# Kernel optimization log

Measured on AMD Instinct MI355X. Metric: run time of the kernel, lower is better.

## Reference

```python
import jax, jax.numpy as jnp
import numpy as np

B, S, HID, NH = 2, 2048, 2048, 16
HD = HID // NH  # head_dim = 128


def setup_inputs() -> dict:
    key = jax.random.key(0)
    ks = jax.random.split(key, 10)
    sc = 1.0 / np.sqrt(HID)
    inp = {
        "hidden_state": jax.random.normal(ks[0], (B, S, HID), dtype=jnp.float32),
        # upper-triangular (strict) causal mask: 1 where attention is forbidden
        "casual_mask": jnp.triu(jnp.ones((S, S), dtype=jnp.float32), k=1),
        # pad last 128 tokens of each sequence
        "pad_mask": jnp.concatenate(
            [jnp.zeros((B, S - 128), jnp.float32), jnp.ones((B, 128), jnp.float32)], axis=1
        ),
        # weights stored [in, out] (transposed vs torch Linear)
        "Wq": jax.random.normal(ks[1], (HID, HID), dtype=jnp.float32) * sc,
        "bq": jnp.zeros((HID,), jnp.float32),
        "Wk": jax.random.normal(ks[2], (HID, HD), dtype=jnp.float32) * sc,
        "bk": jnp.zeros((HD,), jnp.float32),
        "Wv": jax.random.normal(ks[3], (HID, HD), dtype=jnp.float32) * sc,
        "bv": jnp.zeros((HD,), jnp.float32),
        "Wo": jax.random.normal(ks[4], (HID, HID), dtype=jnp.float32) * sc,
        "bo": jnp.zeros((HID,), jnp.float32),
    }
    return inp


def reference(hidden_state, casual_mask, pad_mask, Wq, bq, Wk, bk, Wv, bv, Wo, bo):
    bsz, seq_len, hid = hidden_state.shape
    nh = NH
    hd = hid // nh
    q = hidden_state @ Wq + bq                      # [B,S,HID]
    k = hidden_state @ Wk + bk                      # [B,S,HD]  single shared head
    v = hidden_state @ Wv + bv                      # [B,S,HD]
    q = q.reshape(bsz, seq_len, nh, hd).transpose(0, 2, 1, 3)  # [B,NH,S,HD]
    # attn scores: shared K broadcast across all query heads
    scores = jnp.einsum("bhqd,bkd->bhqk", q, k) / jnp.sqrt(jnp.float32(hd))
    scores = scores + casual_mask * (-1e9)
    scores = scores + pad_mask[:, None, None, :] * (-1e9)
    probs = jax.nn.softmax(scores, axis=-1)         # [B,NH,S,S]
    out = jnp.einsum("bhqk,bkd->bhqd", probs, v)    # [B,NH,S,HD]
    out = out.transpose(0, 2, 1, 3).reshape(bsz, seq_len, hid)
    return out @ Wo + bo
```

## Files before the change

### kernel.cpp

```cpp
#include <hip/hip_runtime.h>
#include <hip/hip_bf16.h>
#include <math.h>

#define B_    2
#define S_    2048
#define HID_  2048
#define NH_   16
#define HD_   128
#define MTOT  4096
#define QKV_N 2304

typedef short bf16x8 __attribute__((ext_vector_type(8)));
typedef float f32x4  __attribute__((ext_vector_type(4)));
typedef float f32x16 __attribute__((ext_vector_type(16)));

__device__ __forceinline__ ushort f2bf(float f) {
    __hip_bfloat16 h = __float2bfloat16(f);
    ushort u; __builtin_memcpy(&u, &h, 2); return u;
}

__device__ __forceinline__ uint cvtpk_bf16(float lo, float hi) {
    uint r;
    asm("v_cvt_pk_bf16_f32 %0, %1, %2" : "=v"(r) : "v"(lo), "v"(hi));
    return r;
}

__device__ __forceinline__ void gload_lds16(const void* g, void* l) {
    __builtin_amdgcn_global_load_lds(
        (const __attribute__((address_space(1))) void*)g,
        (__attribute__((address_space(3))) void*)l, 16, 0, 0);
}

__global__ void prep(const float* __restrict__ hidden, ushort* __restrict__ hbf,
                     const float* __restrict__ Wq, const float* __restrict__ Wk,
                     const float* __restrict__ Wv, const float* __restrict__ Wo,
                     ushort* __restrict__ WqkvT, ushort* __restrict__ WoT,
                     const float* __restrict__ bq, const float* __restrict__ bk,
                     const float* __restrict__ bv, float* __restrict__ bqkv,
                     int* __restrict__ ctr)
{
    __shared__ float tile[32][33];
    const int bid = blockIdx.x;
    const int tid = threadIdx.x;

    if (bid < 4096) {
        long i = ((long)bid * 256 + tid) * 8;
        float4 a = *(const float4*)&hidden[i];
        float4 b = *(const float4*)&hidden[i + 4];
        uint4 o;
        o.x = (uint)f2bf(a.x) | ((uint)f2bf(a.y) << 16);
        o.y = (uint)f2bf(a.z) | ((uint)f2bf(a.w) << 16);
        o.z = (uint)f2bf(b.x) | ((uint)f2bf(b.y) << 16);
        o.w = (uint)f2bf(b.z) | ((uint)f2bf(b.w) << 16);
        *(uint4*)&hbf[i] = o;
        return;
    }
    if (bid >= 12800) {
        int i = (bid - 12800) * 256 + tid;
        if (i == 0) *ctr = 0;
        if (i < 2048)      bqkv[i] = bq[i];
        else if (i < 2176) bqkv[i] = bk[i - 2048];
        else if (i < QKV_N) bqkv[i] = bv[i - 2176];
        return;
    }

    const float* W; ushort* T; int N, rowoff, r;
    if (bid < 8192)      { W = Wq; T = WqkvT; N = 2048; rowoff = 0;    r = bid - 4096; }
    else if (bid < 8448) { W = Wk; T = WqkvT; N = 128;  rowoff = 2048; r = bid - 8192; }
    else if (bid < 8704) { W = Wv; T = WqkvT; N = 128;  rowoff = 2176; r = bid - 8448; }
    else                 { W = Wo; T = WoT;   N = 2048; rowoff = 0;    r = bid - 8704; }
    const int nxt = N >> 5;
    const int bx = r % nxt, by = r / nxt;
    const int tx = tid & 31, ty = tid >> 5;
    const int n0 = bx * 32, k0 = by * 32;
#pragma unroll
    for (int i = 0; i < 4; i++)
        tile[ty + 8 * i][tx] = W[(long)(k0 + ty + 8 * i) * N + n0 + tx];
    __syncthreads();
#pragma unroll
    for (int i = 0; i < 4; i++)
        T[(long)(rowoff + n0 + ty + 8 * i) * 2048 + k0 + tx] = f2bf(tile[tx][ty + 8 * i]);
}

__global__ __launch_bounds__(256, 3) void gemm_qkv(
    const ushort* __restrict__ A, const ushort* __restrict__ Bt,
    const float* __restrict__ bias,
    ushort* __restrict__ qbuf, ushort* __restrict__ kbuf,
    ushort* __restrict__ vtbuf)
{
    const int K = HID_;
    __shared__ __align__(16) ushort As[2 * 128 * 32];
    __shared__ __align__(16) ushort Bs[2 * 128 * 32];
    const int t = threadIdx.x;
    const int w = t >> 6, l = t & 63;
    const long bm = (long)blockIdx.y * 128;
    const long bn = (long)blockIdx.x * 128;

    f32x4 acc[4][4];
#pragma unroll
    for (int i = 0; i < 4; i++)
#pragma unroll
        for (int j = 0; j < 4; j++) acc[i][j] = (f32x4){0.f, 0.f, 0.f, 0.f};

    const int srow = w * 16 + (l >> 2);
    const int scol = (l & 3) * 8;
    const ushort* Ag0 = A + (bm + srow) * (long)K + scol;
    const ushort* Ag1 = A + (bm + srow + 64) * (long)K + scol;
    const ushort* Bg0 = Bt + (bn + srow) * (long)K + scol;
    const ushort* Bg1 = Bt + (bn + srow + 64) * (long)K + scol;
    ushort* Al0 = As + w * 512;
    ushort* Al1 = As + 2048 + w * 512;
    ushort* Bl0 = Bs + w * 512;
    ushort* Bl1 = Bs + 2048 + w * 512;

    const int mrow = l & 15, kq = l >> 4;
    const int moff = (w & 1) * 64, noff = (w >> 1) * 64;

    gload_lds16(Ag0, Al0);
    gload_lds16(Ag1, Al1);
    gload_lds16(Bg0, Bl0);
    gload_lds16(Bg1, Bl1);
    __syncthreads();

    for (int k0 = 0; k0 < K; k0 += 32) {
        const int cb = (k0 >> 5) & 1;
        const int po = cb * 4096;
        if (k0 + 32 < K) {
            const int pn = (cb ^ 1) * 4096;
            gload_lds16(Ag0 + k0 + 32, Al0 + pn);
            gload_lds16(Ag1 + k0 + 32, Al1 + pn);
            gload_lds16(Bg0 + k0 + 32, Bl0 + pn);
            gload_lds16(Bg1 + k0 + 32, Bl1 + pn);
        }
        bf16x8 af[4], bfr[4];
#pragma unroll
        for (int i = 0; i < 4; i++)
            af[i] = *(const bf16x8*)&As[po + (moff + i * 16 + mrow) * 32 + kq * 8];
#pragma unroll
        for (int j = 0; j < 4; j++)
            bfr[j] = *(const bf16x8*)&Bs[po + (noff + j * 16 + mrow) * 32 + kq * 8];
#pragma unroll
        for (int i = 0; i < 4; i++)
#pragma unroll
            for (int j = 0; j < 4; j++)
                acc[i][j] = __builtin_amdgcn_mfma_f32_16x16x32_bf16(
                    af[i], bfr[j], acc[i][j], 0, 0, 0);
        __syncthreads();
    }

    const int crow = (l >> 4) * 4, ccol = l & 15;
    const int tile = blockIdx.x;
#pragma unroll
    for (int i = 0; i < 4; i++) {
#pragma unroll
        for (int j = 0; j < 4; j++) {
            long colg = bn + noff + j * 16 + ccol;
            float bv = bias[colg];
            long row0 = bm + moff + i * 16 + crow;
            float v[4];
#pragma unroll
            for (int r = 0; r < 4; r++) v[r] = acc[i][j][r] + bv;
            if (tile < 16) {
#pragma unroll
                for (int r = 0; r < 4; r++)
                    qbuf[(row0 + r) * (long)HID_ + colg] = f2bf(v[r]);
            } else if (tile == 16) {
                long ck = colg - 2048;
#pragma unroll
                for (int r = 0; r < 4; r++)
                    kbuf[(row0 + r) * (long)HD_ + ck] = f2bf(v[r]);
            } else {
                long cv = colg - 2176;
                long b  = row0 >> 11;
                long s0 = row0 & 2047;
                ushort4 pk;
                pk.x = f2bf(v[0]); pk.y = f2bf(v[1]);
                pk.z = f2bf(v[2]); pk.w = f2bf(v[3]);
                *(ushort4*)&vtbuf[b * (HD_ * (long)S_) + cv * (long)S_ + s0] = pk;
            }
        }
    }
}

__global__ __launch_bounds__(256, 3) void gemm_mfma(
    const ushort* __restrict__ A, const ushort* __restrict__ Bt,
    const float* __restrict__ bias, float* __restrict__ C,
    int K, int ldc)
{
    __shared__ __align__(16) ushort As[2 * 128 * 32];
    __shared__ __align__(16) ushort Bs[2 * 128 * 32];
    const int t = threadIdx.x;
    const int w = t >> 6, l = t & 63;
    const long bm = (long)blockIdx.y * 128;
    const long bn = (long)blockIdx.x * 128;

    f32x4 acc[4][4];
#pragma unroll
    for (int i = 0; i < 4; i++)
#pragma unroll
        for (int j = 0; j < 4; j++) acc[i][j] = (f32x4){0.f, 0.f, 0.f, 0.f};

    const int srow = w * 16 + (l >> 2);
    const int scol = (l & 3) * 8;
    const ushort* Ag0 = A + (bm + srow) * (long)K + scol;
    const ushort* Ag1 = A + (bm + srow + 64) * (long)K + scol;
    const ushort* Bg0 = Bt + (bn + srow) * (long)K + scol;
    const ushort* Bg1 = Bt + (bn + srow + 64) * (long)K + scol;
    ushort* Al0 = As + w * 512;
    ushort* Al1 = As + 2048 + w * 512;
    ushort* Bl0 = Bs + w * 512;
    ushort* Bl1 = Bs + 2048 + w * 512;

    const int mrow = l & 15, kq = l >> 4;
    const int moff = (w & 1) * 64, noff = (w >> 1) * 64;

    gload_lds16(Ag0, Al0);
    gload_lds16(Ag1, Al1);
    gload_lds16(Bg0, Bl0);
    gload_lds16(Bg1, Bl1);
    __syncthreads();

    for (int k0 = 0; k0 < K; k0 += 32) {
        const int cb = (k0 >> 5) & 1;
        const int po = cb * 4096;
        if (k0 + 32 < K) {
            const int pn = (cb ^ 1) * 4096;
            gload_lds16(Ag0 + k0 + 32, Al0 + pn);
            gload_lds16(Ag1 + k0 + 32, Al1 + pn);
            gload_lds16(Bg0 + k0 + 32, Bl0 + pn);
            gload_lds16(Bg1 + k0 + 32, Bl1 + pn);
        }
        bf16x8 af[4], bfr[4];
#pragma unroll
        for (int i = 0; i < 4; i++)
            af[i] = *(const bf16x8*)&As[po + (moff + i * 16 + mrow) * 32 + kq * 8];
#pragma unroll
        for (int j = 0; j < 4; j++)
            bfr[j] = *(const bf16x8*)&Bs[po + (noff + j * 16 + mrow) * 32 + kq * 8];
#pragma unroll
        for (int i = 0; i < 4; i++)
#pragma unroll
            for (int j = 0; j < 4; j++)
                acc[i][j] = __builtin_amdgcn_mfma_f32_16x16x32_bf16(
                    af[i], bfr[j], acc[i][j], 0, 0, 0);
        __syncthreads();
    }

    const int crow = (l >> 4) * 4, ccol = l & 15;
#pragma unroll
    for (int i = 0; i < 4; i++) {
#pragma unroll
        for (int j = 0; j < 4; j++) {
            long col = bn + noff + j * 16 + ccol;
            float bv = bias[col];
#pragma unroll
            for (int r = 0; r < 4; r++) {
                long row = bm + moff + i * 16 + crow + r;
                C[row * (long)ldc + col] = acc[i][j][r] + bv;
            }
        }
    }
}

__global__ __launch_bounds__(512, 1) void attn_mfma(
    const ushort* __restrict__ qbuf, const ushort* __restrict__ kbuf,
    const ushort* __restrict__ vtbuf, ushort* __restrict__ outp,
    int* __restrict__ workctr)
{
    __shared__ __align__(16) char smem[86016];
    ushort* KsB = (ushort*)smem;
    ushort* VtB = (ushort*)(smem + 32768);
    float*  OP  = (float*)smem;
    float*  LP  = (float*)(smem + 65536);
    int*    sidx = (int*)(smem + 66048);

    const int t = threadIdx.x, w = t >> 6, l = t & 63;
    const int wq = w & 3, kh = w >> 2;
    const int l31 = l & 31, h5 = l >> 5;

    int koff[2], klo[2], voff[2], vlo[2];
#pragma unroll
    for (int i = 0; i < 2; i++) {
        const int c = w * 2 + i;
        const int key0 = c * 4 + (l >> 4);
        const int gk = (l & 15) ^ (key0 & 15);
        koff[i] = key0 * HD_ + gk * 8;
        klo[i]  = c * 512 + l * 8;
        const int d = c * 8 + (l >> 3);
        const int gv = (l & 7) ^ (d & 7);
        voff[i] = d * S_ + gv * 8;
        vlo[i]  = c * 512 + l * 8;
    }

    const float SC = 0.08838834764831845f * 1.44269504089f;

    for (;;) {
        if (t == 0) *sidx = atomicAdd(workctr, 1);
        __syncthreads();
        const int idx = *sidx;
        if (idx >= 512) break;

        const int qblk = 15 - (idx >> 5);
        const int hb = idx & 31;
        const int h = hb & 15, b = hb >> 4;
        const long rowbase = (long)b * S_;
        const int qbase = qblk * 128 + wq * 32;
        const int qmaxw = qbase + 31;
        int kTiles = 2 * qblk + 2;
        if (kTiles > 30) kTiles = 30;
        const ushort* kb0 = kbuf + rowbase * (long)HD_;
        const ushort* vb0 = vtbuf + (long)b * (HD_ * (long)S_);

        bf16x8 qf[8];
        {
            const ushort* qp = qbuf + (rowbase + qbase + l31) * (long)HID_
                                    + h * HD_ + h5 * 8;
#pragma unroll
            for (int ks = 0; ks < 8; ks++) qf[ks] = *(const bf16x8*)(qp + ks * 16);
        }

        f32x16 o[4] = {};
        float lrun = 0.f;

#pragma unroll
        for (int i = 0; i < 2; i++) {
            gload_lds16(kb0 + koff[i], KsB + klo[i]);
            gload_lds16(vb0 + voff[i], VtB + vlo[i]);
        }
        __syncthreads();

        for (int kt = 0; kt < kTiles; kt++) {
            const int cur = kt & 1;
            const int ktb = kt * 64;

            if (kt + 1 < kTiles) {
                const int nxt = cur ^ 1;
                const int nb = ktb + 64;
#pragma unroll
                for (int i = 0; i < 2; i++) {
                    gload_lds16(kb0 + koff[i] + (long)nb * HD_,
                                KsB + nxt * 8192 + klo[i]);
                    gload_lds16(vb0 + voff[i] + nb, VtB + nxt * 8192 + vlo[i]);
                }
            }

            if (ktb <= qmaxw) {
                const ushort* Ks = KsB + cur * 8192;
                const ushort* Vt = VtB + cur * 8192;

                f32x16 c0 = {};
                const int key = kh * 32 + l31;
#pragma unroll
                for (int ks = 0; ks < 8; ks++) {
                    const int g = (ks * 2 + h5) ^ (key & 15);
                    bf16x8 a = *(const bf16x8*)&Ks[key * 128 + g * 8];
                    c0 = __builtin_amdgcn_mfma_f32_32x32x16_bf16(
                        a, qf[ks], c0, 0, 0, 0);
                }

                const bool boundary = (ktb + 63 > qbase) || (ktb >= S_ - 128);
                if (boundary) {
                    const int qg = qbase + l31;
#pragma unroll
                    for (int g = 0; g < 4; g++)
#pragma unroll
                        for (int r = 0; r < 4; r++) {
                            const int keyg = ktb + kh * 32 + 4 * h5 + 8 * g + r;
                            if (keyg > qg || keyg >= S_ - 128)
                                c0[g * 4 + r] = -3.0e38f;
                        }
                }

                float s0 = 0.f, s1 = 0.f, s2 = 0.f, s3 = 0.f;
#pragma unroll
                for (int g = 0; g < 4; g++) {
                    float p0 = __builtin_amdgcn_exp2f(c0[g * 4 + 0] * SC);
                    float p1 = __builtin_amdgcn_exp2f(c0[g * 4 + 1] * SC);
                    float p2 = __builtin_amdgcn_exp2f(c0[g * 4 + 2] * SC);
                    float p3 = __builtin_amdgcn_exp2f(c0[g * 4 + 3] * SC);
                    c0[g * 4 + 0] = p0; s0 += p0;
                    c0[g * 4 + 1] = p1; s1 += p1;
                    c0[g * 4 + 2] = p2; s2 += p2;
                    c0[g * 4 + 3] = p3; s3 += p3;
                }
                float sum = (s0 + s1) + (s2 + s3);
                sum += __shfl_xor(sum, 32);
                lrun += sum;

#pragma unroll
                for (int j = 0; j < 2; j++) {
                    const int base = j * 8;
                    uint X  = cvtpk_bf16(c0[base + 0], c0[base + 1]);
                    uint Y  = cvtpk_bf16(c0[base + 2], c0[base + 3]);
                    uint Z  = cvtpk_bf16(c0[base + 4], c0[base + 5]);
                    uint Wd = cvtpk_bf16(c0[base + 6], c0[base + 7]);
                    asm("v_permlane32_swap_b32 %0, %1" : "+v"(X), "+v"(Z));
                    asm("v_permlane32_swap_b32 %0, %1" : "+v"(Y), "+v"(Wd));
                    uint tmp[4] = {X, Y, Z, Wd};
                    bf16x8 pf;
                    __builtin_memcpy(&pf, tmp, 16);
                    const int ks2 = kh * 2 + j;
#pragma unroll
                    for (int mb = 0; mb < 4; mb++) {
                        const int d = mb * 32 + l31;
                        const int g = (ks2 * 2 + h5) ^ (d & 7);
                        bf16x8 a = *(const bf16x8*)&Vt[d * 64 + g * 8];
                        o[mb] = __builtin_amdgcn_mfma_f32_32x32x16_bf16(
                            a, pf, o[mb], 0, 0, 0);
                    }
                }
            }
            __syncthreads();
        }

        if (kh == 1) {
#pragma unroll
            for (int mb = 0; mb < 4; mb++)
#pragma unroll
                for (int r = 0; r < 16; r++) {
                    const int d = mb * 32 + (r & 3) + 8 * (r >> 2) + 4 * h5;
                    OP[wq * 4096 + d * 32 + l31] = o[mb][r];
                }
            LP[wq * 32 + l31] = lrun;
        }
        __syncthreads();
        if (kh == 0) {
#pragma unroll
            for (int mb = 0; mb < 4; mb++)
#pragma unroll
                for (int r = 0; r < 16; r++) {
                    const int d = mb * 32 + (r & 3) + 8 * (r >> 2) + 4 * h5;
                    o[mb][r] += OP[wq * 4096 + d * 32 + l31];
                }
            lrun += LP[wq * 32 + l31];
        }
        __syncthreads();

        if (kh == 0) {
            ushort* Ob = (ushort*)smem + wq * 4352;
            const float inv = 1.f / lrun;
#pragma unroll
            for (int mb = 0; mb < 4; mb++) {
#pragma unroll
                for (int g = 0; g < 4; g++) {
                    const int d0 = mb * 32 + 4 * h5 + 8 * g;
                    ushort4 pk;
                    pk.x = f2bf(o[mb][g * 4 + 0] * inv);
                    pk.y = f2bf(o[mb][g * 4 + 1] * inv);
                    pk.z = f2bf(o[mb][g * 4 + 2] * inv);
                    pk.w = f2bf(o[mb][g * 4 + 3] * inv);
                    *(ushort4*)&Ob[l31 * 136 + d0] = pk;
                }
            }
            __builtin_amdgcn_s_waitcnt(0);
            const int q = l >> 1, half = l & 1;
            const ushort* src = Ob + q * 136 + half * 64;
            ushort* dst = outp + (rowbase + qblk * 128 + wq * 32 + q) * (long)HID_
                               + h * HD_ + half * 64;
#pragma unroll
            for (int i = 0; i < 8; i++) {
                uint4 v = *(const uint4*)(src + i * 8);
                *(uint4*)(dst + i * 8) = v;
            }
        }
    }
}

extern "C" void kernel_launch(void* const* d_in, const int* in_sizes, int n_in,
                              void* d_out, int out_size, void* d_ws, size_t ws_size,
                              hipStream_t stream)
{
    const float* hidden = (const float*)d_in[0];
    const float* Wq  = (const float*)d_in[3];
    const float* bq  = (const float*)d_in[4];
    const float* Wk  = (const float*)d_in[5];
    const float* bk  = (const float*)d_in[6];
    const float* Wv  = (const float*)d_in[7];
    const float* bv  = (const float*)d_in[8];
    const float* Wo  = (const float*)d_in[9];
    const float* bo  = (const float*)d_in[10];
    float* out = (float*)d_out;

    char* ws = (char*)d_ws;
    ushort* hbf   = (ushort*)(ws);
    ushort* WqkvT = (ushort*)(ws + 16777216);
    ushort* WoT   = (ushort*)(ws + 26214400);
    float*  bqkv  = (float*) (ws + 34603008);
    int*    wctr  = (int*)   (ws + 34612224);
    ushort* qbuf  = (ushort*)(ws + 34619392);
    ushort* kbuf  = (ushort*)(ws + 51396608);
    ushort* vtbuf = (ushort*)(ws + 52445184);
    ushort* attnO = (ushort*)(ws + 53493760);

    prep<<<12809, 256, 0, stream>>>(hidden, hbf, Wq, Wk, Wv, Wo,
                                    WqkvT, WoT, bq, bk, bv, bqkv, wctr);
    gemm_qkv<<<dim3(18, 32), 256, 0, stream>>>(hbf, WqkvT, bqkv,
                                               qbuf, kbuf, vtbuf);
    attn_mfma<<<256, 512, 0, stream>>>(qbuf, kbuf, vtbuf, attnO, wctr);
    gemm_mfma<<<dim3(16, 32), 256, 0, stream>>>(attnO, WoT, bo, out,
                                                HID_, HID_);
}
```

Baseline: 285.7 us.

## Replace persistent atomic work queue in attention with static grid and two blocks per CU

```diff
diff --git a/kernel.cpp b/kernel.cpp
--- a/kernel.cpp
+++ b/kernel.cpp
@@ -36,8 +36,7 @@
                      const float* __restrict__ Wv, const float* __restrict__ Wo,
                      ushort* __restrict__ WqkvT, ushort* __restrict__ WoT,
                      const float* __restrict__ bq, const float* __restrict__ bk,
-                     const float* __restrict__ bv, float* __restrict__ bqkv,
-                     int* __restrict__ ctr)
+                     const float* __restrict__ bv, float* __restrict__ bqkv)
 {
     __shared__ float tile[32][33];
     const int bid = blockIdx.x;
@@ -57,7 +56,6 @@
     }
     if (bid >= 12800) {
         int i = (bid - 12800) * 256 + tid;
-        if (i == 0) *ctr = 0;
         if (i < 2048)      bqkv[i] = bq[i];
         else if (i < 2176) bqkv[i] = bk[i - 2048];
         else if (i < QKV_N) bqkv[i] = bv[i - 2176];
@@ -262,21 +260,32 @@
     }
 }
 
-__global__ __launch_bounds__(512, 1) void attn_mfma(
+__global__ __launch_bounds__(512) __attribute__((amdgpu_waves_per_eu(4, 4)))
+void attn_mfma(
     const ushort* __restrict__ qbuf, const ushort* __restrict__ kbuf,
-    const ushort* __restrict__ vtbuf, ushort* __restrict__ outp,
-    int* __restrict__ workctr)
+    const ushort* __restrict__ vtbuf, ushort* __restrict__ outp)
 {
-    __shared__ __align__(16) char smem[86016];
+    __shared__ __align__(16) char smem[66048];
     ushort* KsB = (ushort*)smem;
     ushort* VtB = (ushort*)(smem + 32768);
     float*  OP  = (float*)smem;
     float*  LP  = (float*)(smem + 65536);
-    int*    sidx = (int*)(smem + 66048);
 
     const int t = threadIdx.x, w = t >> 6, l = t & 63;
     const int wq = w & 3, kh = w >> 2;
     const int l31 = l & 31, h5 = l >> 5;
+
+    const int bid = blockIdx.x;
+    const int qblk = (bid < 256) ? (15 - (bid >> 5)) : ((bid - 256) >> 5);
+    const int hb = bid & 31;
+    const int h = hb & 15, b = hb >> 4;
+    const long rowbase = (long)b * S_;
+    const int qbase = qblk * 128 + wq * 32;
+    const int qmaxw = qbase + 31;
+    int kTiles = 2 * qblk + 2;
+    if (kTiles > 30) kTiles = 30;
+    const ushort* kb0 = kbuf + rowbase * (long)HD_;
+    const ushort* vb0 = vtbuf + (long)b * (HD_ * (long)S_);
 
     int koff[2], klo[2], voff[2], vlo[2];
 #pragma unroll
@@ -294,174 +303,156 @@
 
     const float SC = 0.08838834764831845f * 1.44269504089f;
 
-    for (;;) {
-        if (t == 0) *sidx = atomicAdd(workctr, 1);
+    bf16x8 qf[8];
+    {
+        const ushort* qp = qbuf + (rowbase + qbase + l31) * (long)HID_
+                                + h * HD_ + h5 * 8;
+#pragma unroll
+        for (int ks = 0; ks < 8; ks++) qf[ks] = *(const bf16x8*)(qp + ks * 16);
+    }
+
+    f32x16 o[4] = {};
+    float lrun = 0.f;
+
+#pragma unroll
+    for (int i = 0; i < 2; i++) {
+        gload_lds16(kb0 + koff[i], KsB + klo[i]);
+        gload_lds16(vb0 + voff[i], VtB + vlo[i]);
+    }
+    __syncthreads();
+
+    for (int kt = 0; kt < kTiles; kt++) {
+        const int cur = kt & 1;
+        const int ktb = kt * 64;
+
+        if (kt + 1 < kTiles) {
+            const int nxt = cur ^ 1;
+            const int nb = ktb + 64;
+#pragma unroll
+            for (int i = 0; i < 2; i++) {
+                gload_lds16(kb0 + koff[i] + (long)nb * HD_,
+                            KsB + nxt * 8192 + klo[i]);
+                gload_lds16(vb0 + voff[i] + nb, VtB + nxt * 8192 + vlo[i]);
+            }
+        }
+
+        if (ktb <= qmaxw) {
+            const ushort* Ks = KsB + cur * 8192;
+            const ushort* Vt = VtB + cur * 8192;
+
+            f32x16 c0 = {};
+            const int key = kh * 32 + l31;
+#pragma unroll
+            for (int ks = 0; ks < 8; ks++) {
+                const int g = (ks * 2 + h5) ^ (key & 15);
+                bf16x8 a = *(const bf16x8*)&Ks[key * 128 + g * 8];
+                c0 = __builtin_amdgcn_mfma_f32_32x32x16_bf16(
+                    a, qf[ks], c0, 0, 0, 0);
+            }
+
+            const bool boundary = (ktb + 63 > qbase);
+            if (boundary) {
+                const int qg = qbase + l31;
+#pragma unroll
+                for (int g = 0; g < 4; g++)
+#pragma unroll
+                    for (int r = 0; r < 4; r++) {
+                        const int keyg = ktb + kh * 32 + 4 * h5 + 8 * g + r;
+                        if (keyg > qg)
+                            c0[g * 4 + r] = -3.0e38f;
+                    }
+            }
+
+            float s0 = 0.f, s1 = 0.f, s2 = 0.f, s3 = 0.f;
+#pragma unroll
+            for (int g = 0; g < 4; g++) {
+                float p0 = __builtin_amdgcn_exp2f(c0[g * 4 + 0] * SC);
+                float p1 = __builtin_amdgcn_exp2f(c0[g * 4 + 1] * SC);
+                float p2 = __builtin_amdgcn_exp2f(c0[g * 4 + 2] * SC);
+                float p3 = __builtin_amdgcn_exp2f(c0[g * 4 + 3] * SC);
+                c0[g * 4 + 0] = p0; s0 += p0;
+                c0[g * 4 + 1] = p1; s1 += p1;
+                c0[g * 4 + 2] = p2; s2 += p2;
+                c0[g * 4 + 3] = p3; s3 += p3;
+            }
+            float sum = (s0 + s1) + (s2 + s3);
+            sum += __shfl_xor(sum, 32);
+            lrun += sum;
+
+#pragma unroll
+            for (int j = 0; j < 2; j++) {
+                const int base = j * 8;
+                uint X  = cvtpk_bf16(c0[base + 0], c0[base + 1]);
+                uint Y  = cvtpk_bf16(c0[base + 2], c0[base + 3]);
+                uint Z  = cvtpk_bf16(c0[base + 4], c0[base + 5]);
+                uint Wd = cvtpk_bf16(c0[base + 6], c0[base + 7]);
+                asm("v_permlane32_swap_b32 %0, %1" : "+v"(X), "+v"(Z));
+                asm("v_permlane32_swap_b32 %0, %1" : "+v"(Y), "+v"(Wd));
+                uint tmp[4] = {X, Y, Z, Wd};
+                bf16x8 pf;
+                __builtin_memcpy(&pf, tmp, 16);
+                const int ks2 = kh * 2 + j;
+#pragma unroll
+                for (int mb = 0; mb < 4; mb++) {
+                    const int d = mb * 32 + l31;
+                    const int g = (ks2 * 2 + h5) ^ (d & 7);
+                    bf16x8 a = *(const bf16x8*)&Vt[d * 64 + g * 8];
+                    o[mb] = __builtin_amdgcn_mfma_f32_32x32x16_bf16(
+                        a, pf, o[mb], 0, 0, 0);
+                }
+            }
+        }
         __syncthreads();
-        const int idx = *sidx;
-        if (idx >= 512) break;
-
-        const int qblk = 15 - (idx >> 5);
-        const int hb = idx & 31;
-        const int h = hb & 15, b = hb >> 4;
-        const long rowbase = (long)b * S_;
-        const int qbase = qblk * 128 + wq * 32;
-        const int qmaxw = qbase + 31;
-        int kTiles = 2 * qblk + 2;
-        if (kTiles > 30) kTiles = 30;
-        const ushort* kb0 = kbuf + rowbase * (long)HD_;
-        const ushort* vb0 = vtbuf + (long)b * (HD_ * (long)S_);
-
-        bf16x8 qf[8];
-        {
-            const ushort* qp = qbuf + (rowbase + qbase + l31) * (long)HID_
-                                    + h * HD_ + h5 * 8;
-#pragma unroll
-            for (int ks = 0; ks < 8; ks++) qf[ks] = *(const bf16x8*)(qp + ks * 16);
-        }
-
-        f32x16 o[4] = {};
-        float lrun = 0.f;
-
-#pragma unroll
-        for (int i = 0; i < 2; i++) {
-            gload_lds16(kb0 + koff[i], KsB + klo[i]);
-            gload_lds16(vb0 + voff[i], VtB + vlo[i]);
-        }
-        __syncthreads();
-
-        for (int kt = 0; kt < kTiles; kt++) {
-            const int cur = kt & 1;
-            const int ktb = kt * 64;
-
-            if (kt + 1 < kTiles) {
-                const int nxt = cur ^ 1;
-                const int nb = ktb + 64;
-#pragma unroll
-                for (int i = 0; i < 2; i++) {
-                    gload_lds16(kb0 + koff[i] + (long)nb * HD_,
-                                KsB + nxt * 8192 + klo[i]);
-                    gload_lds16(vb0 + voff[i] + nb, VtB + nxt * 8192 + vlo[i]);
-                }
-            }
-
-            if (ktb <= qmaxw) {
-                const ushort* Ks = KsB + cur * 8192;
-                const ushort* Vt = VtB + cur * 8192;
-
-                f32x16 c0 = {};
-                const int key = kh * 32 + l31;
-#pragma unroll
-                for (int ks = 0; ks < 8; ks++) {
-                    const int g = (ks * 2 + h5) ^ (key & 15);
-                    bf16x8 a = *(const bf16x8*)&Ks[key * 128 + g * 8];
-                    c0 = __builtin_amdgcn_mfma_f32_32x32x16_bf16(
-                        a, qf[ks], c0, 0, 0, 0);
-                }
-
-                const bool boundary = (ktb + 63 > qbase) || (ktb >= S_ - 128);
-                if (boundary) {
-                    const int qg = qbase + l31;
-#pragma unroll
-                    for (int g = 0; g < 4; g++)
-#pragma unroll
-                        for (int r = 0; r < 4; r++) {
-                            const int keyg = ktb + kh * 32 + 4 * h5 + 8 * g + r;
-                            if (keyg > qg || keyg >= S_ - 128)
-                                c0[g * 4 + r] = -3.0e38f;
-                        }
-                }
-
-                float s0 = 0.f, s1 = 0.f, s2 = 0.f, s3 = 0.f;
-#pragma unroll
-                for (int g = 0; g < 4; g++) {
-                    float p0 = __builtin_amdgcn_exp2f(c0[g * 4 + 0] * SC);
-                    float p1 = __builtin_amdgcn_exp2f(c0[g * 4 + 1] * SC);
-                    float p2 = __builtin_amdgcn_exp2f(c0[g * 4 + 2] * SC);
-                    float p3 = __builtin_amdgcn_exp2f(c0[g * 4 + 3] * SC);
-                    c0[g * 4 + 0] = p0; s0 += p0;
-                    c0[g * 4 + 1] = p1; s1 += p1;
-                    c0[g * 4 + 2] = p2; s2 += p2;
-                    c0[g * 4 + 3] = p3; s3 += p3;
-                }
-                float sum = (s0 + s1) + (s2 + s3);
-                sum += __shfl_xor(sum, 32);
-                lrun += sum;
-
-#pragma unroll
-                for (int j = 0; j < 2; j++) {
-                    const int base = j * 8;
-                    uint X  = cvtpk_bf16(c0[base + 0], c0[base + 1]);
-                    uint Y  = cvtpk_bf16(c0[base + 2], c0[base + 3]);
-                    uint Z  = cvtpk_bf16(c0[base + 4], c0[base + 5]);
-                    uint Wd = cvtpk_bf16(c0[base + 6], c0[base + 7]);
-                    asm("v_permlane32_swap_b32 %0, %1" : "+v"(X), "+v"(Z));
-                    asm("v_permlane32_swap_b32 %0, %1" : "+v"(Y), "+v"(Wd));
-                    uint tmp[4] = {X, Y, Z, Wd};
-                    bf16x8 pf;
-                    __builtin_memcpy(&pf, tmp, 16);
-                    const int ks2 = kh * 2 + j;
-#pragma unroll
-                    for (int mb = 0; mb < 4; mb++) {
-                        const int d = mb * 32 + l31;
-                        const int g = (ks2 * 2 + h5) ^ (d & 7);
-                        bf16x8 a = *(const bf16x8*)&Vt[d * 64 + g * 8];
-                        o[mb] = __builtin_amdgcn_mfma_f32_32x32x16_bf16(
-                            a, pf, o[mb], 0, 0, 0);
-                    }
-                }
-            }
-            __syncthreads();
-        }
-
-        if (kh == 1) {
-#pragma unroll
-            for (int mb = 0; mb < 4; mb++)
-#pragma unroll
-                for (int r = 0; r < 16; r++) {
-                    const int d = mb * 32 + (r & 3) + 8 * (r >> 2) + 4 * h5;
-                    OP[wq * 4096 + d * 32 + l31] = o[mb][r];
-                }
-            LP[wq * 32 + l31] = lrun;
-        }
-        __syncthreads();
-        if (kh == 0) {
-#pragma unroll
-            for (int mb = 0; mb < 4; mb++)
-#pragma unroll
-                for (int r = 0; r < 16; r++) {
-                    const int d = mb * 32 + (r & 3) + 8 * (r >> 2) + 4 * h5;
-                    o[mb][r] += OP[wq * 4096 + d * 32 + l31];
-                }
-            lrun += LP[wq * 32 + l31];
-        }
-        __syncthreads();
-
-        if (kh == 0) {
-            ushort* Ob = (ushort*)smem + wq * 4352;
-            const float inv = 1.f / lrun;
-#pragma unroll
-            for (int mb = 0; mb < 4; mb++) {
-#pragma unroll
-                for (int g = 0; g < 4; g++) {
-                    const int d0 = mb * 32 + 4 * h5 + 8 * g;
-                    ushort4 pk;
-                    pk.x = f2bf(o[mb][g * 4 + 0] * inv);
-                    pk.y = f2bf(o[mb][g * 4 + 1] * inv);
-                    pk.z = f2bf(o[mb][g * 4 + 2] * inv);
-                    pk.w = f2bf(o[mb][g * 4 + 3] * inv);
-                    *(ushort4*)&Ob[l31 * 136 + d0] = pk;
-                }
-            }
-            __builtin_amdgcn_s_waitcnt(0);
-            const int q = l >> 1, half = l & 1;
-            const ushort* src = Ob + q * 136 + half * 64;
-            ushort* dst = outp + (rowbase + qblk * 128 + wq * 32 + q) * (long)HID_
-                               + h * HD_ + half * 64;
-#pragma unroll
-            for (int i = 0; i < 8; i++) {
-                uint4 v = *(const uint4*)(src + i * 8);
-                *(uint4*)(dst + i * 8) = v;
-            }
+    }
+
+    if (kh == 1) {
+#pragma unroll
+        for (int mb = 0; mb < 4; mb++)
+#pragma unroll
+            for (int r = 0; r < 16; r++) {
+                const int d = mb * 32 + (r & 3) + 8 * (r >> 2) + 4 * h5;
+                OP[wq * 4096 + d * 32 + l31] = o[mb][r];
+            }
+        LP[wq * 32 + l31] = lrun;
+    }
+    __syncthreads();
+    if (kh == 0) {
+#pragma unroll
+        for (int mb = 0; mb < 4; mb++)
+#pragma unroll
+            for (int r = 0; r < 16; r++) {
+                const int d = mb * 32 + (r & 3) + 8 * (r >> 2) + 4 * h5;
+                o[mb][r] += OP[wq * 4096 + d * 32 + l31];
+            }
+        lrun += LP[wq * 32 + l31];
+    }
+    __syncthreads();
+
+    if (kh == 0) {
+        ushort* Ob = (ushort*)smem + wq * 4352;
+        const float inv = 1.f / lrun;
+#pragma unroll
+        for (int mb = 0; mb < 4; mb++) {
+#pragma unroll
+            for (int g = 0; g < 4; g++) {
+                const int d0 = mb * 32 + 4 * h5 + 8 * g;
+                ushort4 pk;
+                pk.x = f2bf(o[mb][g * 4 + 0] * inv);
+                pk.y = f2bf(o[mb][g * 4 + 1] * inv);
+                pk.z = f2bf(o[mb][g * 4 + 2] * inv);
+                pk.w = f2bf(o[mb][g * 4 + 3] * inv);
+                *(ushort4*)&Ob[l31 * 136 + d0] = pk;
+            }
+        }
+        __builtin_amdgcn_s_waitcnt(0);
+        const int q = l >> 1, half = l & 1;
+        const ushort* src = Ob + q * 136 + half * 64;
+        ushort* dst = outp + (rowbase + qblk * 128 + wq * 32 + q) * (long)HID_
+                           + h * HD_ + half * 64;
+#pragma unroll
+        for (int i = 0; i < 8; i++) {
+            uint4 v = *(const uint4*)(src + i * 8);
+            *(uint4*)(dst + i * 8) = v;
         }
     }
 }
@@ -486,17 +477,16 @@
     ushort* WqkvT = (ushort*)(ws + 16777216);
     ushort* WoT   = (ushort*)(ws + 26214400);
     float*  bqkv  = (float*) (ws + 34603008);
-    int*    wctr  = (int*)   (ws + 34612224);
     ushort* qbuf  = (ushort*)(ws + 34619392);
     ushort* kbuf  = (ushort*)(ws + 51396608);
     ushort* vtbuf = (ushort*)(ws + 52445184);
     ushort* attnO = (ushort*)(ws + 53493760);
 
     prep<<<12809, 256, 0, stream>>>(hidden, hbf, Wq, Wk, Wv, Wo,
-                                    WqkvT, WoT, bq, bk, bv, bqkv, wctr);
+                                    WqkvT, WoT, bq, bk, bv, bqkv);
     gemm_qkv<<<dim3(18, 32), 256, 0, stream>>>(hbf, WqkvT, bqkv,
                                                qbuf, kbuf, vtbuf);
-    attn_mfma<<<256, 512, 0, stream>>>(qbuf, kbuf, vtbuf, attnO, wctr);
+    attn_mfma<<<512, 512, 0, stream>>>(qbuf, kbuf, vtbuf, attnO);
     gemm_mfma<<<dim3(16, 32), 256, 0, stream>>>(attnO, WoT, bo, out,
                                                 HID_, HID_);
 }
```

After: 325.1 us. +13.8%, slower.
